# Optimization experiments

Hardware: AMD Instinct MI355X
Metric: run time of the kernel (lower is better)

Reference implementation:

```python
import jax, jax.numpy as jnp
import numpy as np
from functools import partial

SR = 60
DT = 1.0 / SR
N_JOINTS = 8


def setup_inputs() -> dict:
    key = jax.random.key(0)
    k1, k2, k3, k4, k5 = jax.random.split(key, 5)
    B, T = 1024, 2048
    # x packs [F_flex, F_ext, K_flex, K_ext] per joint -> input_size = 4*n_joints
    x = jax.random.uniform(k1, (B, T, 4 * N_JOINTS), dtype=jnp.float32)
    # joint state: (theta, d_theta) per joint
    state0 = jax.random.normal(k2, (B, N_JOINTS, 2), dtype=jnp.float32) * 0.1
    # moment arms for 2 antagonistic muscles per joint
    M = jax.random.normal(k3, (N_JOINTS, 2), dtype=jnp.float32) * 0.02
    inertia = jax.random.uniform(k4, (N_JOINTS,), dtype=jnp.float32) * 0.01 + 0.005
    damping = jax.random.uniform(k5, (N_JOINTS,), dtype=jnp.float32) * 0.05 + 0.01
    return {"x": x, "state0": state0, "M": M, "inertia": inertia, "damping": damping}


def reference(x, state0, M, inertia, damping):
    B, T, _ = x.shape
    xr = x.reshape(B, T, N_JOINTS, 4)
    F = xr[..., :2]  # [B, T, J, 2] muscle forces
    K = xr[..., 2:]  # [B, T, J, 2] muscle stiffnesses
    M2 = M * M  # [J, 2]

    def step(carry, inp):
        theta, dtheta = carry  # each [B, J]
        F_t, K_t = inp  # each [B, J, 2]
        # joint torque: active muscle torque - stiffness restoring torque - viscous damping
        tau = (jnp.einsum('jm,bjm->bj', M, F_t)
               - theta * jnp.einsum('jm,bjm->bj', M2, K_t)
               - damping * dtheta)
        ddtheta = tau / inertia
        dtheta = dtheta + ddtheta * DT  # semi-implicit Euler
        theta = theta + dtheta * DT
        return (theta, dtheta), theta

    F_s = jnp.moveaxis(F, 1, 0)  # [T, B, J, 2]
    K_s = jnp.moveaxis(K, 1, 0)
    (theta_T, dtheta_T), out = jax.lax.scan(step, (state0[..., 0], state0[..., 1]), (F_s, K_s))
    out = jnp.moveaxis(out, 0, 1)  # [B, T, J]
    final_state = jnp.stack([theta_T, dtheta_T], axis=2)  # [B, J, 2]
    # muscle states = joint state projected through moment arms [B, J, 2, 2]
    muscle_states = final_state[..., None] * M[None, :, None, :]
    return out, muscle_states, final_state
```

## Files before the change

### kernel.cpp

```cpp
#include <hip/hip_runtime.h>

#define NJ 8
#define TS 2048
#define NB 1024
#define JW 4
#define CHUNK 256
#define NCH (TS / CHUNK)
#define F4C (CHUNK * JW)
#define DTC (1.0f / 60.0f)

__device__ __forceinline__ void dma16(const float4* g, float4* lds_base) {
#if __has_builtin(__builtin_amdgcn_global_load_lds)
    __builtin_amdgcn_global_load_lds(
        (const __attribute__((address_space(1))) void*)g,
        (__attribute__((address_space(3))) void*)lds_base,
        16, 0, 0);
#else
    lds_base[threadIdx.x & 63] = *g;
#endif
}

template<int CTRL>
__device__ __forceinline__ float dppf(float v) {
    return __int_as_float(__builtin_amdgcn_update_dpp(
        __float_as_int(v), __float_as_int(v), CTRL, 0xF, 0xF, false));
}

#define ROUND(CTRL, COND) do {                                          \
    float o_r0 = dppf<CTRL>(r0), o_r1 = dppf<CTRL>(r1),                 \
          o_rc = dppf<CTRL>(rc), o_s0 = dppf<CTRL>(s0),                 \
          o_s1 = dppf<CTRL>(s1), o_sc = dppf<CTRL>(sc);                 \
    if (COND) {                                                         \
        float nr0 = fmaf(r0, o_s0, r1 * o_r0);                          \
        float nr1 = fmaf(r0, o_s1, r1 * o_r1);                          \
        float nrc = fmaf(r0, o_sc, fmaf(r1, o_rc, rc));                 \
        float ns0 = fmaf(s0, o_s0, s1 * o_r0);                          \
        float ns1 = fmaf(s0, o_s1, s1 * o_r1);                          \
        float nsc = fmaf(s0, o_sc, fmaf(s1, o_rc, sc));                 \
        r0 = nr0; r1 = nr1; rc = nrc; s0 = ns0; s1 = ns1; sc = nsc;     \
    } } while (0)

__global__ __launch_bounds__(256, 4) void phys_dpp_kernel(
    const float4* __restrict__ x,
    const float*  __restrict__ state0,
    const float*  __restrict__ M,
    const float*  __restrict__ inertia,
    const float*  __restrict__ damping,
    float* __restrict__ out,
    float* __restrict__ muscle,
    float* __restrict__ finals)
{
    __shared__ float4 xin[2][F4C];
    __shared__ float4 tb[2][CHUNK * JW / 4];

    const int g   = blockIdx.x;
    const int b   = (g & 7) | ((g >> 4) << 3);
    const int J0  = ((g >> 3) & 1) * JW;

    const int tid  = threadIdx.x;
    const int w    = tid >> 6;
    const int lane = tid & 63;
    const int j    = J0 + w;

    const float M0  = M[j * 2 + 0];
    const float M1  = M[j * 2 + 1];
    const float M20 = M0 * M0;
    const float M21 = M1 * M1;
    const float d   = damping[j];
    const float p   = DTC / inertia[j];
    const float gd  = 1.0f - p * d;

    float thc  = state0[(b * NJ + j) * 2 + 0];
    float dthc = state0[(b * NJ + j) * 2 + 1];

    const float4* xb = x + (size_t)b * TS * NJ;

    auto issue = [&](int ch, float4* bb) {
        const int T0 = ch * CHUNK;
        #pragma unroll
        for (int i = 0; i < 4; ++i) {
            int dd = 256 * w + 64 * i + lane;
            int n  = dd ^ ((dd >> 4) & 7);
            const float4* src = xb + (size_t)(T0 + (n >> 2)) * NJ + J0 + (n & 3);
            dma16(src, bb + 256 * w + 64 * i);
        }
    };

    issue(0, xin[0]);

    for (int ch = 0; ch <= NCH; ++ch) {
        __syncthreads();

        if (ch + 1 < NCH) issue(ch + 1, xin[(ch + 1) & 1]);

        if (ch > 0) {
            const float4* tr = tb[(ch - 1) & 1];
            int f  = tid;
            int q  = f ^ ((f >> 5) & 7);
            int pm = (f >> 3) & 3;
            float4 r = tr[q];
            float rx = r.x, ry = r.y, rz = r.z, rw = r.w;
            if (pm & 1) { float tq = rx; rx = ry; ry = tq; tq = rz; rz = rw; rw = tq; }
            if (pm & 2) { float tq = rx; rx = rz; rz = tq; tq = ry; ry = rw; rw = tq; }
            float4* og = (float4*)out
                       + 2 * ((size_t)b * TS + (size_t)(ch - 1) * CHUNK + f)
                       + (J0 >> 2);
            *og = make_float4(rx, ry, rz, rw);
        }

        if (ch < NCH) {
            const float4* xc = xin[ch & 1];
            float* tw = (float*)tb[ch & 1];

            float a[4], cc[4];
            const int bm = lane & 7;
            #pragma unroll
            for (int k = 0; k < 4; ++k) {
                int n = 16 * lane + 4 * k + w;
                float4 v = xc[n ^ bm];
                a[k]  = fmaf(M0,  v.x, M1  * v.y);
                cc[k] = fmaf(M20, v.z, M21 * v.w);
            }

            float r0 = 0.0f, r1 = 1.0f, rc = 0.0f;
            float s0 = 1.0f, s1 = 0.0f, sc = 0.0f;
            #pragma unroll
            for (int k = 0; k < 4; ++k) {
                float pa = p * a[k];
                float pc = p * cc[k];
                float nr0 = fmaf(-pc, s0, gd * r0);
                float nr1 = fmaf(-pc, s1, gd * r1);
                float nrc = fmaf(-pc, sc, fmaf(gd, rc, pa));
                s0 = fmaf(DTC, nr0, s0);
                s1 = fmaf(DTC, nr1, s1);
                sc = fmaf(DTC, nrc, sc);
                r0 = nr0; r1 = nr1; rc = nrc;
            }

            ROUND(0x111, (lane & 15) >= 1);
            ROUND(0x112, (lane & 15) >= 2);
            ROUND(0x114, (lane & 15) >= 4);
            ROUND(0x118, (lane & 15) >= 8);
            ROUND(0x142, (lane & 31) >= 16);
            ROUND(0x143, lane >= 32);

            float th_e  = fmaf(s0, thc, fmaf(s1, dthc, sc));
            float dth_e = fmaf(r0, thc, fmaf(r1, dthc, rc));
            float th  = __shfl_up(th_e, 1, 64);
            float dth = __shfl_up(dth_e, 1, 64);
            if (lane == 0) { th = thc; dth = dthc; }

            const int wsig = (lane >> 1) & 31;
            #pragma unroll
            for (int k = 0; k < 4; ++k) {
                float u = fmaf(-cc[k], th, a[k]);
                u = fmaf(-d, dth, u);
                dth = fmaf(p, u, dth);
                th  = fmaf(DTC, dth, th);
                tw[(16 * lane + 4 * k + w) ^ wsig] = th;
            }

            thc  = __shfl(th, 63, 64);
            dthc = __shfl(dth, 63, 64);
        }
    }

    if (lane == 0) {
        const int idx = b * NJ + j;
        finals[idx * 2 + 0] = thc;
        finals[idx * 2 + 1] = dthc;
        muscle[idx * 4 + 0] = thc  * M0;
        muscle[idx * 4 + 1] = thc  * M1;
        muscle[idx * 4 + 2] = dthc * M0;
        muscle[idx * 4 + 3] = dthc * M1;
    }
}

extern "C" void kernel_launch(void* const* d_in, const int* in_sizes, int n_in,
                              void* d_out, int out_size, void* d_ws, size_t ws_size,
                              hipStream_t stream) {
    const float4* x      = (const float4*)d_in[0];
    const float*  state0 = (const float*)d_in[1];
    const float*  M      = (const float*)d_in[2];
    const float*  inertia= (const float*)d_in[3];
    const float*  damping= (const float*)d_in[4];

    float* out    = (float*)d_out;
    float* muscle = out + (size_t)NB * TS * NJ;
    float* finals = muscle + (size_t)NB * NJ * 2 * 2;

    dim3 block(256);
    dim3 grid(NB * 2);
    phys_dpp_kernel<<<grid, block, 0, stream>>>(x, state0, M, inertia, damping,
                                                out, muscle, finals);
}
```

Measured before the change: 72.24 us.

## Load inputs directly to registers and process all joints per block

```diff
diff --git a/kernel.cpp b/kernel.cpp
--- a/kernel.cpp
+++ b/kernel.cpp
@@ -3,22 +3,9 @@
 #define NJ 8
 #define TS 2048
 #define NB 1024
-#define JW 4
 #define CHUNK 256
 #define NCH (TS / CHUNK)
-#define F4C (CHUNK * JW)
 #define DTC (1.0f / 60.0f)
-
-__device__ __forceinline__ void dma16(const float4* g, float4* lds_base) {
-#if __has_builtin(__builtin_amdgcn_global_load_lds)
-    __builtin_amdgcn_global_load_lds(
-        (const __attribute__((address_space(1))) void*)g,
-        (__attribute__((address_space(3))) void*)lds_base,
-        16, 0, 0);
-#else
-    lds_base[threadIdx.x & 63] = *g;
-#endif
-}
 
 template<int CTRL>
 __device__ __forceinline__ float dppf(float v) {
@@ -40,7 +27,13 @@
         r0 = nr0; r1 = nr1; rc = nrc; s0 = ns0; s1 = ns1; sc = nsc;     \
     } } while (0)
 
-__global__ __launch_bounds__(256, 4) void phys_dpp_kernel(
+__device__ __forceinline__ void lgkm_barrier() {
+    asm volatile("s_waitcnt lgkmcnt(0)" ::: "memory");
+    __builtin_amdgcn_s_barrier();
+    __builtin_amdgcn_sched_barrier(0);
+}
+
+__global__ __launch_bounds__(512, 4) void phys_direct_kernel(
     const float4* __restrict__ x,
     const float*  __restrict__ state0,
     const float*  __restrict__ M,
@@ -50,17 +43,12 @@
     float* __restrict__ muscle,
     float* __restrict__ finals)
 {
-    __shared__ float4 xin[2][F4C];
-    __shared__ float4 tb[2][CHUNK * JW / 4];
+    __shared__ float4 tb[2][CHUNK * NJ / 4];
 
-    const int g   = blockIdx.x;
-    const int b   = (g & 7) | ((g >> 4) << 3);
-    const int J0  = ((g >> 3) & 1) * JW;
-
+    const int b    = blockIdx.x;
     const int tid  = threadIdx.x;
-    const int w    = tid >> 6;
+    const int j    = tid >> 6;
     const int lane = tid & 63;
-    const int j    = J0 + w;
 
     const float M0  = M[j * 2 + 0];
     const float M1  = M[j * 2 + 1];
@@ -74,50 +62,42 @@
     float dthc = state0[(b * NJ + j) * 2 + 1];
 
     const float4* xb = x + (size_t)b * TS * NJ;
+    const int lbase = 32 * lane + j;
 
-    auto issue = [&](int ch, float4* bb) {
-        const int T0 = ch * CHUNK;
-        #pragma unroll
-        for (int i = 0; i < 4; ++i) {
-            int dd = 256 * w + 64 * i + lane;
-            int n  = dd ^ ((dd >> 4) & 7);
-            const float4* src = xb + (size_t)(T0 + (n >> 2)) * NJ + J0 + (n & 3);
-            dma16(src, bb + 256 * w + 64 * i);
-        }
-    };
+    float4 cv[4], nv[4];
+    #pragma unroll
+    for (int k = 0; k < 4; ++k) cv[k] = xb[lbase + 8 * k];
 
-    issue(0, xin[0]);
+    float4* outf4 = (float4*)out + (size_t)b * TS * 2;
 
     for (int ch = 0; ch <= NCH; ++ch) {
-        __syncthreads();
+        lgkm_barrier();
 
-        if (ch + 1 < NCH) issue(ch + 1, xin[(ch + 1) & 1]);
+        if (ch + 1 < NCH) {
+            #pragma unroll
+            for (int k = 0; k < 4; ++k)
+                nv[k] = xb[(ch + 1) * (CHUNK * NJ) + lbase + 8 * k];
+        }
 
         if (ch > 0) {
             const float4* tr = tb[(ch - 1) & 1];
             int f  = tid;
-            int q  = f ^ ((f >> 5) & 7);
-            int pm = (f >> 3) & 3;
-            float4 r = tr[q];
+            int m  = (f >> 4) & 31;
+            int pm = m & 3;
+            float4 r = tr[f ^ (m >> 2)];
             float rx = r.x, ry = r.y, rz = r.z, rw = r.w;
             if (pm & 1) { float tq = rx; rx = ry; ry = tq; tq = rz; rz = rw; rw = tq; }
             if (pm & 2) { float tq = rx; rx = rz; rz = tq; tq = ry; ry = rw; rw = tq; }
-            float4* og = (float4*)out
-                       + 2 * ((size_t)b * TS + (size_t)(ch - 1) * CHUNK + f)
-                       + (J0 >> 2);
-            *og = make_float4(rx, ry, rz, rw);
+            outf4[(size_t)(ch - 1) * (CHUNK / 2) * 4 + f] = make_float4(rx, ry, rz, rw);
         }
 
         if (ch < NCH) {
-            const float4* xc = xin[ch & 1];
             float* tw = (float*)tb[ch & 1];
 
             float a[4], cc[4];
-            const int bm = lane & 7;
             #pragma unroll
             for (int k = 0; k < 4; ++k) {
-                int n = 16 * lane + 4 * k + w;
-                float4 v = xc[n ^ bm];
+                float4 v = cv[k];
                 a[k]  = fmaf(M0,  v.x, M1  * v.y);
                 cc[k] = fmaf(M20, v.z, M21 * v.w);
             }
@@ -157,11 +137,14 @@
                 u = fmaf(-d, dth, u);
                 dth = fmaf(p, u, dth);
                 th  = fmaf(DTC, dth, th);
-                tw[(16 * lane + 4 * k + w) ^ wsig] = th;
+                tw[(32 * lane + 8 * k + j) ^ wsig] = th;
             }
 
             thc  = __shfl(th, 63, 64);
             dthc = __shfl(dth, 63, 64);
+
+            #pragma unroll
+            for (int k = 0; k < 4; ++k) cv[k] = nv[k];
         }
     }
 
@@ -189,8 +172,8 @@
     float* muscle = out + (size_t)NB * TS * NJ;
     float* finals = muscle + (size_t)NB * NJ * 2 * 2;
 
-    dim3 block(256);
-    dim3 grid(NB * 2);
-    phys_dpp_kernel<<<grid, block, 0, stream>>>(x, state0, M, inertia, damping,
-                                                out, muscle, finals);
+    dim3 block(512);
+    dim3 grid(NB);
+    phys_direct_kernel<<<grid, block, 0, stream>>>(x, state0, M, inertia, damping,
+                                                   out, muscle, finals);
 }
```

Result: slower. 78.45 us (+8.6%).
